# Kernel tuning notes

Measured on AMD Instinct MI355X. Metric: run time of the kernel, lower is better.

## Reference

```python
import jax, jax.numpy as jnp
import numpy as np

HEADS = 16
HEAD_DIM = 64
EMBED = HEADS * HEAD_DIM  # 1024
B, S = 2, 2048


def setup_inputs() -> dict:
    key = jax.random.key(0)
    ks = jax.random.split(key, 9)
    return {
        "value": jax.random.normal(ks[0], (B, S, EMBED), dtype=jnp.float32),
        "key": jax.random.normal(ks[1], (B, S, EMBED), dtype=jnp.float32),
        "query": jax.random.normal(ks[2], (B, S, EMBED), dtype=jnp.float32),
        "mask": jax.random.randint(ks[3], (B, 1, S, S), 0, 2, dtype=jnp.int32),
        "Wq": jax.random.normal(ks[4], (HEAD_DIM, HEAD_DIM), dtype=jnp.float32) * 0.02,
        "Wk": jax.random.normal(ks[5], (HEAD_DIM, HEAD_DIM), dtype=jnp.float32) * 0.02,
        "Wv": jax.random.normal(ks[6], (HEAD_DIM, HEAD_DIM), dtype=jnp.float32) * 0.02,
        "Wo": jax.random.normal(ks[7], (EMBED, EMBED), dtype=jnp.float32) * 0.02,
        "bo": jnp.zeros((EMBED,), dtype=jnp.float32),
    }


def reference(value, key, query, mask, Wq, Wk, Wv, Wo, bo):
    N, Lv = value.shape[0], value.shape[1]
    Lk, Lq = key.shape[1], query.shape[1]
    # Faithful to original: plain reshape (N, heads, len, head_dim), NOT transpose.
    v = value.reshape(N, HEADS, Lv, HEAD_DIM)
    k = key.reshape(N, HEADS, Lk, HEAD_DIM)
    q = query.reshape(N, HEADS, Lq, HEAD_DIM)
    # Per-head Linear (no bias): x @ W.T
    V = jnp.einsum('bhld,ed->bhle', v, Wv)
    K = jnp.einsum('bhld,ed->bhle', k, Wk)
    Q = jnp.einsum('bhld,ed->bhle', q, Wq)
    score = jnp.einsum('bhqd,bhkd->bhqk', Q, K)  # [B,H,Sq,Sk]
    score = jnp.where(mask == 0, jnp.float32(-1e20), score)
    # Faithful quirk: scale by sqrt(embed_size), not sqrt(head_dim)
    scale = jnp.float32(EMBED ** 0.5)
    attn = jax.nn.softmax(score / scale, axis=3)
    out = jnp.einsum('bhqk,bhkd->bhqd', attn, V).reshape(N, Lq, HEADS * HEAD_DIM)
    return out @ Wo.T + bo
```

## Files before the change

kernel.cpp:

```cpp
#include <hip/hip_runtime.h>
#include <hip/hip_bf16.h>
#include <cstdint>
#include <cstddef>

#define S_LEN 2048
#define N_HEADS 16
#define HD 64
#define EMB 1024
#define N_BATCH 2
#define N_BH (N_BATCH * N_HEADS)

typedef __attribute__((ext_vector_type(4))) float f32x4;
typedef __attribute__((ext_vector_type(8))) short short8;
typedef __attribute__((ext_vector_type(8))) _Float16 half8;
typedef __attribute__((ext_vector_type(2))) _Float16 half2v;

__device__ __forceinline__ f32x4 mfma16h(half8 a, half8 b, f32x4 c) {
    return __builtin_amdgcn_mfma_f32_16x16x32_f16(a, b, c, 0, 0, 0);
}

__device__ __forceinline__ unsigned pkh(float a, float b) {
    return __builtin_bit_cast(unsigned, __builtin_amdgcn_cvt_pkrtz(a, b));
}

#if __has_builtin(__builtin_amdgcn_exp2f)
__device__ __forceinline__ float fast_exp2(float x) { return __builtin_amdgcn_exp2f(x); }
#else
__device__ __forceinline__ float fast_exp2(float x) { return exp2f(x); }
#endif

__global__ __launch_bounds__(256) void prep_kernel(
    const float* __restrict__ q_in, const float* __restrict__ k_in,
    const float* __restrict__ v_in,
    const float* __restrict__ Wq, const float* __restrict__ Wk,
    const float* __restrict__ Wv, const float* __restrict__ Wo,
    const int* __restrict__ mask,
    short* __restrict__ Qb, short* __restrict__ Kb, short* __restrict__ Vt,
    short* __restrict__ Woh, unsigned long long* __restrict__ bits) {
    __shared__ short Al[64 * 72];
    __shared__ short Wl[64 * 72];
    __shared__ short Ol[64 * 72];
    int bx = blockIdx.x;
    int t = threadIdx.x;

    if (bx >= 3072) {
        if (bx < 11264) {
            int wid = ((bx - 3072) * 256 + t) >> 6;
            int lane = t & 63;
            const int* src = mask + (size_t)wid * 256 + lane;
            unsigned long long w0 = __ballot(src[0] != 0);
            unsigned long long w1 = __ballot(src[64] != 0);
            unsigned long long w2 = __ballot(src[128] != 0);
            unsigned long long w3 = __ballot(src[192] != 0);
            if (lane == 0) {
                unsigned long long* dst = bits + (size_t)wid * 4;
                dst[0] = w0; dst[1] = w1; dst[2] = w2; dst[3] = w3;
            }
        } else {
            int i = (bx - 11264) * 256 + t;
            f32x4 a = reinterpret_cast<const f32x4*>(Wo)[i * 2];
            f32x4 b = reinterpret_cast<const f32x4*>(Wo)[i * 2 + 1];
            uint4 u = { pkh(a.x, a.y), pkh(a.z, a.w), pkh(b.x, b.y), pkh(b.z, b.w) };
            reinterpret_cast<uint4*>(Woh)[i] = u;
        }
        return;
    }

    int rt = bx & 31;
    int bh = (bx >> 5) & 31;
    int tz = bx >> 10;
    const float* src = (tz == 0 ? q_in : tz == 1 ? k_in : v_in)
                       + (size_t)bh * S_LEN * HD + (size_t)rt * 64 * HD;
    const float* W = (tz == 0 ? Wq : tz == 1 ? Wk : Wv);

#pragma unroll
    for (int r = 0; r < 4; r++) {
        int f4 = t + 256 * r;
        int row = f4 >> 4;
        int c4 = (f4 & 15) * 4;
        f32x4 a = reinterpret_cast<const f32x4*>(src)[f4];
        uint2 ua = { pkh(a.x, a.y), pkh(a.z, a.w) };
        *reinterpret_cast<uint2*>(&Al[row * 72 + c4]) = ua;
        f32x4 w = reinterpret_cast<const f32x4*>(W)[f4];
        uint2 uw = { pkh(w.x, w.y), pkh(w.z, w.w) };
        *reinterpret_cast<uint2*>(&Wl[row * 72 + c4]) = uw;
    }
    __syncthreads();

    int wave = t >> 6, lane = t & 63, quad = lane >> 4, col = lane & 15;
    half8 a0 = *reinterpret_cast<const half8*>(&Al[(wave * 16 + col) * 72 + quad * 8]);
    half8 a1 = *reinterpret_cast<const half8*>(&Al[(wave * 16 + col) * 72 + 32 + quad * 8]);

    const float C1 = 0.04508422002777448f;
    float scl = (tz == 0) ? C1 : 1.0f;

    f32x4 acc[4];
#pragma unroll
    for (int jt = 0; jt < 4; jt++) {
        half8 b0 = *reinterpret_cast<const half8*>(&Wl[(jt * 16 + col) * 72 + quad * 8]);
        half8 b1 = *reinterpret_cast<const half8*>(&Wl[(jt * 16 + col) * 72 + 32 + quad * 8]);
        f32x4 c = {0.f, 0.f, 0.f, 0.f};
        c = mfma16h(a0, b0, c);
        c = mfma16h(a1, b1, c);
        acc[jt] = c;
    }
    __syncthreads();

    if (tz < 2) {
#pragma unroll
        for (int jt = 0; jt < 4; jt++)
#pragma unroll
            for (int i = 0; i < 4; i++)
                Ol[(wave * 16 + quad * 4 + i) * 72 + jt * 16 + col] =
                    __builtin_bit_cast(short, (_Float16)(acc[jt][i] * scl));
        __syncthreads();
        short* dst = (tz == 0 ? Qb : Kb) + (size_t)bh * S_LEN * HD + (size_t)rt * 64 * HD;
        int row = t >> 2, ck = (t & 3) * 16;
        short8 o0 = *reinterpret_cast<const short8*>(&Ol[row * 72 + ck]);
        short8 o1 = *reinterpret_cast<const short8*>(&Ol[row * 72 + ck + 8]);
        *reinterpret_cast<short8*>(&dst[row * 64 + ck]) = o0;
        *reinterpret_cast<short8*>(&dst[row * 64 + ck + 8]) = o1;
    } else {
#pragma unroll
        for (int jt = 0; jt < 4; jt++)
#pragma unroll
            for (int i = 0; i < 4; i++)
                Ol[(jt * 16 + col) * 72 + wave * 16 + quad * 4 + i] =
                    __builtin_bit_cast(short, (_Float16)acc[jt][i]);
        __syncthreads();
        short* dst = Vt + (size_t)bh * HD * S_LEN + rt * 64;
        int d = t >> 2, ck = (t & 3) * 16;
        short8 o0 = *reinterpret_cast<const short8*>(&Ol[d * 72 + ck]);
        short8 o1 = *reinterpret_cast<const short8*>(&Ol[d * 72 + ck + 8]);
        *reinterpret_cast<short8*>(&dst[(size_t)d * S_LEN + ck]) = o0;
        *reinterpret_cast<short8*>(&dst[(size_t)d * S_LEN + ck + 8]) = o1;
    }
}

__global__ __launch_bounds__(512, 4) void attn_kernel(
    const short* __restrict__ Qb, const short* __restrict__ Kb,
    const short* __restrict__ Vt, const unsigned long long* __restrict__ mbits,
    short* __restrict__ Xb) {
    int qt = blockIdx.x;
    int bh = blockIdx.y;
    int b = bh >> 4;
    int t = threadIdx.x, wave = t >> 6, lane = t & 63, quad = lane >> 4, col = lane & 15;

    __shared__ short Ks[64 * 64];
    __shared__ short Vs[64 * 64];
    __shared__ short Pl[8][16 * 72];
    short* Pw = &Pl[wave][0];

    const short* Qh = Qb + (size_t)bh * S_LEN * HD;
    const short* Kh = Kb + (size_t)bh * S_LEN * HD;
    const short* Vh = Vt + (size_t)bh * HD * S_LEN;
    int q0w = qt * 128 + wave * 16;
    int q = q0w + col;

    half8 qf0 = *reinterpret_cast<const half8*>(&Qh[(size_t)q * HD + quad * 8]);
    half8 qf1 = *reinterpret_cast<const half8*>(&Qh[(size_t)q * HD + 32 + quad * 8]);
    const unsigned long long* mrow = mbits + (size_t)(b * S_LEN + q) * 32;

    int r0 = t >> 3, cc = t & 7;
    int dst0 = r0 * 64 + ((cc ^ (r0 & 7)) * 8);
    const short* kg0 = Kh + r0 * HD + cc * 8;
    const short* vg0 = Vh + (size_t)r0 * S_LEN + cc * 8;

    short8 pk0 = *reinterpret_cast<const short8*>(kg0);
    short8 pv0 = *reinterpret_cast<const short8*>(vg0);
    *reinterpret_cast<short8*>(&Ks[dst0]) = pk0;
    *reinterpret_cast<short8*>(&Vs[dst0]) = pv0;
    __syncthreads();

    unsigned bs[4];
#pragma unroll
    for (int i = 0; i < 4; i++) bs[i] = 1u << (quad * 4 + i);
    half8 ones = { (_Float16)1.f, (_Float16)1.f, (_Float16)1.f, (_Float16)1.f,
                   (_Float16)1.f, (_Float16)1.f, (_Float16)1.f, (_Float16)1.f };

    int sw = quad ^ (col & 7);
    unsigned long long mw = mrow[0];

    f32x4 o[4];
    f32x4 l = {0.f, 0.f, 0.f, 0.f};
#pragma unroll
    for (int dt = 0; dt < 4; dt++) o[dt] = (f32x4){0.f, 0.f, 0.f, 0.f};

    for (int kt = 0; kt < 32; kt++) {
        unsigned long long mw_n;
        if (kt < 31) {
            pk0 = *reinterpret_cast<const short8*>(kg0 + (kt + 1) * 4096);
            pv0 = *reinterpret_cast<const short8*>(vg0 + (kt + 1) * 64);
            mw_n = mrow[kt + 1];
        }
        f32x4 s[4];
#pragma unroll
        for (int mt = 0; mt < 4; mt++) {
            const short* kbase = &Ks[(mt * 16 + col) * 64];
            half8 ka0 = *reinterpret_cast<const half8*>(&kbase[sw * 8]);
            half8 ka1 = *reinterpret_cast<const half8*>(&kbase[(sw ^ 4) * 8]);
            f32x4 c = {0.f, 0.f, 0.f, 0.f};
            c = mfma16h(ka0, qf0, c);
            c = mfma16h(ka1, qf1, c);
            s[mt] = c;
        }
#pragma unroll
        for (int mt = 0; mt < 4; mt++) {
            unsigned g = (unsigned)(mw >> (mt * 16));
            float p0 = fast_exp2((g & bs[0]) ? s[mt][0] : -200.0f);
            float p1 = fast_exp2((g & bs[1]) ? s[mt][1] : -200.0f);
            float p2 = fast_exp2((g & bs[2]) ? s[mt][2] : -200.0f);
            float p3 = fast_exp2((g & bs[3]) ? s[mt][3] : -200.0f);
            uint2 dw = { pkh(p0, p1), pkh(p2, p3) };
            *reinterpret_cast<uint2*>(&Pw[col * 72 + mt * 16 + quad * 4]) = dw;
        }
#pragma unroll
        for (int c = 0; c < 2; c++) {
            half8 pb = *reinterpret_cast<const half8*>(&Pw[col * 72 + c * 32 + quad * 8]);
            l = mfma16h(ones, pb, l);
#pragma unroll
            for (int dt = 0; dt < 4; dt++) {
                half8 va = *reinterpret_cast<const half8*>(
                    &Vs[(dt * 16 + col) * 64 + (((c * 4 + quad) ^ (col & 7)) * 8)]);
                o[dt] = mfma16h(va, pb, o[dt]);
            }
        }
        __syncthreads();
        if (kt < 31) {
            *reinterpret_cast<short8*>(&Ks[dst0]) = pk0;
            *reinterpret_cast<short8*>(&Vs[dst0]) = pv0;
            mw = mw_n;
            __syncthreads();
        }
    }

    float inv = 1.0f / l[0];
#pragma unroll
    for (int dt = 0; dt < 4; dt++) {
        uint2 dw = { pkh(o[dt][0] * inv, o[dt][1] * inv),
                     pkh(o[dt][2] * inv, o[dt][3] * inv) };
        *reinterpret_cast<uint2*>(&Pw[col * 72 + dt * 16 + quad * 4]) = dw;
    }
    int rr = lane >> 2, ck = (lane & 3) * 16;
    short8 x0 = *reinterpret_cast<const short8*>(&Pw[rr * 72 + ck]);
    short8 x1 = *reinterpret_cast<const short8*>(&Pw[rr * 72 + ck + 8]);
    short* Xrow = Xb + (size_t)bh * S_LEN * HD + (size_t)(q0w + rr) * HD;
    *reinterpret_cast<short8*>(&Xrow[ck]) = x0;
    *reinterpret_cast<short8*>(&Xrow[ck + 8]) = x1;
}

__global__ __launch_bounds__(256, 4) void final_kernel(
    const short* __restrict__ Xb, const short* __restrict__ Woh,
    const float* __restrict__ bo, float* __restrict__ out) {
    int nb = blockIdx.x;
    int mb = blockIdx.y;
    int t = threadIdx.x, wave = t >> 6, lane = t & 63, quad = lane >> 4, col = lane & 15;
    __shared__ short Xs[64 * 64];
    __shared__ short Ws[64 * 64];
    __shared__ float Olds[64 * 68];

    int m0 = mb * 64, n0 = nb * 64;
    int r0 = t >> 3, r1 = (t + 256) >> 3, cc = t & 7;
    int dst0 = r0 * 64 + ((cc ^ (r0 & 7)) * 8);
    int dst1 = r1 * 64 + ((cc ^ (r1 & 7)) * 8);
    const short* xg0 = Xb + (size_t)(m0 + r0) * EMB + cc * 8;
    const short* xg1 = Xb + (size_t)(m0 + r1) * EMB + cc * 8;
    const short* wg0 = Woh + (size_t)(n0 + r0) * EMB + cc * 8;
    const short* wg1 = Woh + (size_t)(n0 + r1) * EMB + cc * 8;

    short8 px0 = *reinterpret_cast<const short8*>(xg0);
    short8 px1 = *reinterpret_cast<const short8*>(xg1);
    short8 pw0 = *reinterpret_cast<const short8*>(wg0);
    short8 pw1 = *reinterpret_cast<const short8*>(wg1);
    *reinterpret_cast<short8*>(&Xs[dst0]) = px0;
    *reinterpret_cast<short8*>(&Xs[dst1]) = px1;
    *reinterpret_cast<short8*>(&Ws[dst0]) = pw0;
    *reinterpret_cast<short8*>(&Ws[dst1]) = pw1;
    __syncthreads();

    int sw = quad ^ (col & 7);
    f32x4 acc[4];
#pragma unroll
    for (int jt = 0; jt < 4; jt++) acc[jt] = (f32x4){0.f, 0.f, 0.f, 0.f};

    for (int s = 0; s < 16; s++) {
        if (s < 15) {
            px0 = *reinterpret_cast<const short8*>(xg0 + (s + 1) * 64);
            px1 = *reinterpret_cast<const short8*>(xg1 + (s + 1) * 64);
            pw0 = *reinterpret_cast<const short8*>(wg0 + (s + 1) * 64);
            pw1 = *reinterpret_cast<const short8*>(wg1 + (s + 1) * 64);
        }
        const short* arow = &Xs[(wave * 16 + col) * 64];
        half8 a0 = *reinterpret_cast<const half8*>(&arow[sw * 8]);
        half8 a1 = *reinterpret_cast<const half8*>(&arow[(sw ^ 4) * 8]);
#pragma unroll
        for (int jt = 0; jt < 4; jt++) {
            const short* brow = &Ws[(jt * 16 + col) * 64];
            half8 b0 = *reinterpret_cast<const half8*>(&brow[sw * 8]);
            half8 b1 = *reinterpret_cast<const half8*>(&brow[(sw ^ 4) * 8]);
            acc[jt] = mfma16h(a0, b0, acc[jt]);
            acc[jt] = mfma16h(a1, b1, acc[jt]);
        }
        __syncthreads();
        if (s < 15) {
            *reinterpret_cast<short8*>(&Xs[dst0]) = px0;
            *reinterpret_cast<short8*>(&Xs[dst1]) = px1;
            *reinterpret_cast<short8*>(&Ws[dst0]) = pw0;
            *reinterpret_cast<short8*>(&Ws[dst1]) = pw1;
            __syncthreads();
        }
    }

#pragma unroll
    for (int jt = 0; jt < 4; jt++)
#pragma unroll
        for (int i = 0; i < 4; i++)
            Olds[(wave * 16 + quad * 4 + i) * 68 + jt * 16 + col] = acc[jt][i];
    __syncthreads();
    int row = t >> 2, ck = (t & 3) * 16;
#pragma unroll
    for (int u = 0; u < 4; u++) {
        f32x4 v = *reinterpret_cast<const f32x4*>(&Olds[row * 68 + ck + u * 4]);
        f32x4 bb = *reinterpret_cast<const f32x4*>(&bo[n0 + ck + u * 4]);
        v.x += bb.x; v.y += bb.y; v.z += bb.z; v.w += bb.w;
        *reinterpret_cast<f32x4*>(&out[(size_t)(m0 + row) * EMB + n0 + ck + u * 4]) = v;
    }
}

extern "C" void kernel_launch(void* const* d_in, const int* in_sizes, int n_in,
                              void* d_out, int out_size, void* d_ws, size_t ws_size,
                              hipStream_t stream) {
    const float* value = (const float*)d_in[0];
    const float* key_  = (const float*)d_in[1];
    const float* query = (const float*)d_in[2];
    const int*   mask  = (const int*)d_in[3];
    const float* Wq = (const float*)d_in[4];
    const float* Wk = (const float*)d_in[5];
    const float* Wv = (const float*)d_in[6];
    const float* Wo = (const float*)d_in[7];
    const float* bo = (const float*)d_in[8];
    float* out = (float*)d_out;

    char* ws = (char*)d_ws;
    short* Qb  = (short*)(ws);
    short* Kb  = (short*)(ws + (size_t)8  * 1048576);
    short* Vt  = (short*)(ws + (size_t)16 * 1048576);
    short* Xb  = (short*)(ws + (size_t)24 * 1048576);
    short* Woh = (short*)(ws + (size_t)32 * 1048576);
    unsigned long long* mbits =
        (unsigned long long*)(ws + (size_t)34 * 1048576);

    prep_kernel<<<dim3(3072 + 8192 + 512), dim3(256), 0, stream>>>(
        query, key_, value, Wq, Wk, Wv, Wo, mask, Qb, Kb, Vt, Woh, mbits);
    attn_kernel<<<dim3(S_LEN / 128, N_BH), dim3(512), 0, stream>>>(Qb, Kb, Vt, mbits, Xb);
    final_kernel<<<dim3(EMB / 64, (N_BATCH * S_LEN) / 64), dim3(256), 0, stream>>>(
        Xb, Woh, bo, out);
}
```

Measured before the change: 205.8 us.

## Split KV tiles across wave halves with 32-row query tiles per wave

The attention kernel now gives each wave 32 query rows (two 16-row MFMA tiles) so every K and V fragment read from LDS feeds twice as many MFMAs. The 8 waves are split into two parity groups that process alternating 64-key tiles, with two K/V tiles staged per sync. The partial outputs and row sums are merged through shared memory at the end. This is meant to halve LDS traffic per FLOP and halve the number of barriers, at the cost of more registers, a larger shared-memory footprint, and a final cross-wave reduction.

```diff
diff --git a/kernel.cpp b/kernel.cpp
--- a/kernel.cpp
+++ b/kernel.cpp
@@ -145,31 +145,43 @@
     int bh = blockIdx.y;
     int b = bh >> 4;
     int t = threadIdx.x, wave = t >> 6, lane = t & 63, quad = lane >> 4, col = lane & 15;
-
-    __shared__ short Ks[64 * 64];
-    __shared__ short Vs[64 * 64];
-    __shared__ short Pl[8][16 * 72];
-    short* Pw = &Pl[wave][0];
+    int qg = wave & 3;
+    int par = wave >> 2;
+
+    __shared__ short smem[16384 + 8 * 32 * 72];
+    short* Pl = smem + 16384;
+    short* Pw = Pl + wave * (32 * 72);
+    const short* Kp = smem + par * 4096;
+    const short* Vp = smem + 8192 + par * 4096;
 
     const short* Qh = Qb + (size_t)bh * S_LEN * HD;
     const short* Kh = Kb + (size_t)bh * S_LEN * HD;
     const short* Vh = Vt + (size_t)bh * HD * S_LEN;
-    int q0w = qt * 128 + wave * 16;
-    int q = q0w + col;
-
-    half8 qf0 = *reinterpret_cast<const half8*>(&Qh[(size_t)q * HD + quad * 8]);
-    half8 qf1 = *reinterpret_cast<const half8*>(&Qh[(size_t)q * HD + 32 + quad * 8]);
-    const unsigned long long* mrow = mbits + (size_t)(b * S_LEN + q) * 32;
+    int q0 = qt * 128 + qg * 32;
+
+    half8 qf00 = *reinterpret_cast<const half8*>(&Qh[(size_t)(q0 + col) * HD + quad * 8]);
+    half8 qf01 = *reinterpret_cast<const half8*>(&Qh[(size_t)(q0 + col) * HD + 32 + quad * 8]);
+    half8 qf10 = *reinterpret_cast<const half8*>(&Qh[(size_t)(q0 + 16 + col) * HD + quad * 8]);
+    half8 qf11 = *reinterpret_cast<const half8*>(&Qh[(size_t)(q0 + 16 + col) * HD + 32 + quad * 8]);
+
+    const unsigned long long* mrow0 = mbits + (size_t)(b * S_LEN + q0 + col) * 32;
+    const unsigned long long* mrow1 = mbits + (size_t)(b * S_LEN + q0 + 16 + col) * 32;
 
     int r0 = t >> 3, cc = t & 7;
     int dst0 = r0 * 64 + ((cc ^ (r0 & 7)) * 8);
     const short* kg0 = Kh + r0 * HD + cc * 8;
     const short* vg0 = Vh + (size_t)r0 * S_LEN + cc * 8;
 
-    short8 pk0 = *reinterpret_cast<const short8*>(kg0);
-    short8 pv0 = *reinterpret_cast<const short8*>(vg0);
-    *reinterpret_cast<short8*>(&Ks[dst0]) = pk0;
-    *reinterpret_cast<short8*>(&Vs[dst0]) = pv0;
+    {
+        short8 a = *reinterpret_cast<const short8*>(kg0);
+        short8 b2 = *reinterpret_cast<const short8*>(kg0 + 4096);
+        short8 c = *reinterpret_cast<const short8*>(vg0);
+        short8 d = *reinterpret_cast<const short8*>(vg0 + 64);
+        *reinterpret_cast<short8*>(&smem[dst0]) = a;
+        *reinterpret_cast<short8*>(&smem[4096 + dst0]) = b2;
+        *reinterpret_cast<short8*>(&smem[8192 + dst0]) = c;
+        *reinterpret_cast<short8*>(&smem[12288 + dst0]) = d;
+    }
     __syncthreads();
 
     unsigned bs[4];
@@ -179,74 +191,124 @@
                    (_Float16)1.f, (_Float16)1.f, (_Float16)1.f, (_Float16)1.f };
 
     int sw = quad ^ (col & 7);
-    unsigned long long mw = mrow[0];
-
-    f32x4 o[4];
-    f32x4 l = {0.f, 0.f, 0.f, 0.f};
-#pragma unroll
-    for (int dt = 0; dt < 4; dt++) o[dt] = (f32x4){0.f, 0.f, 0.f, 0.f};
-
-    for (int kt = 0; kt < 32; kt++) {
-        unsigned long long mw_n;
-        if (kt < 31) {
-            pk0 = *reinterpret_cast<const short8*>(kg0 + (kt + 1) * 4096);
-            pv0 = *reinterpret_cast<const short8*>(vg0 + (kt + 1) * 64);
-            mw_n = mrow[kt + 1];
-        }
-        f32x4 s[4];
+    unsigned long long mw0 = mrow0[par];
+    unsigned long long mw1 = mrow1[par];
+
+    f32x4 o[4][2];
+    f32x4 l0 = {0.f, 0.f, 0.f, 0.f}, l1 = {0.f, 0.f, 0.f, 0.f};
+#pragma unroll
+    for (int dt = 0; dt < 4; dt++) {
+        o[dt][0] = (f32x4){0.f, 0.f, 0.f, 0.f};
+        o[dt][1] = (f32x4){0.f, 0.f, 0.f, 0.f};
+    }
+
+    for (int s = 0; s < 16; s++) {
+        short8 pk0, pk1, pv0, pv1;
+        unsigned long long mn0, mn1;
+        if (s < 15) {
+            pk0 = *reinterpret_cast<const short8*>(kg0 + (2 * s + 2) * 4096);
+            pk1 = *reinterpret_cast<const short8*>(kg0 + (2 * s + 3) * 4096);
+            pv0 = *reinterpret_cast<const short8*>(vg0 + (2 * s + 2) * 64);
+            pv1 = *reinterpret_cast<const short8*>(vg0 + (2 * s + 3) * 64);
+            mn0 = mrow0[2 * s + 2 + par];
+            mn1 = mrow1[2 * s + 2 + par];
+        }
 #pragma unroll
         for (int mt = 0; mt < 4; mt++) {
-            const short* kbase = &Ks[(mt * 16 + col) * 64];
+            const short* kbase = &Kp[(mt * 16 + col) * 64];
             half8 ka0 = *reinterpret_cast<const half8*>(&kbase[sw * 8]);
             half8 ka1 = *reinterpret_cast<const half8*>(&kbase[(sw ^ 4) * 8]);
-            f32x4 c = {0.f, 0.f, 0.f, 0.f};
-            c = mfma16h(ka0, qf0, c);
-            c = mfma16h(ka1, qf1, c);
-            s[mt] = c;
-        }
-#pragma unroll
-        for (int mt = 0; mt < 4; mt++) {
-            unsigned g = (unsigned)(mw >> (mt * 16));
-            float p0 = fast_exp2((g & bs[0]) ? s[mt][0] : -200.0f);
-            float p1 = fast_exp2((g & bs[1]) ? s[mt][1] : -200.0f);
-            float p2 = fast_exp2((g & bs[2]) ? s[mt][2] : -200.0f);
-            float p3 = fast_exp2((g & bs[3]) ? s[mt][3] : -200.0f);
-            uint2 dw = { pkh(p0, p1), pkh(p2, p3) };
-            *reinterpret_cast<uint2*>(&Pw[col * 72 + mt * 16 + quad * 4]) = dw;
+            f32x4 c0 = {0.f, 0.f, 0.f, 0.f};
+            f32x4 c1 = {0.f, 0.f, 0.f, 0.f};
+            c0 = mfma16h(ka0, qf00, c0);
+            c0 = mfma16h(ka1, qf01, c0);
+            c1 = mfma16h(ka0, qf10, c1);
+            c1 = mfma16h(ka1, qf11, c1);
+            unsigned g0 = (unsigned)(mw0 >> (mt * 16));
+            unsigned g1 = (unsigned)(mw1 >> (mt * 16));
+            float p00 = fast_exp2((g0 & bs[0]) ? c0[0] : -200.0f);
+            float p01 = fast_exp2((g0 & bs[1]) ? c0[1] : -200.0f);
+            float p02 = fast_exp2((g0 & bs[2]) ? c0[2] : -200.0f);
+            float p03 = fast_exp2((g0 & bs[3]) ? c0[3] : -200.0f);
+            uint2 dw0 = { pkh(p00, p01), pkh(p02, p03) };
+            *reinterpret_cast<uint2*>(&Pw[col * 72 + mt * 16 + quad * 4]) = dw0;
+            float p10 = fast_exp2((g1 & bs[0]) ? c1[0] : -200.0f);
+            float p11 = fast_exp2((g1 & bs[1]) ? c1[1] : -200.0f);
+            float p12 = fast_exp2((g1 & bs[2]) ? c1[2] : -200.0f);
+            float p13 = fast_exp2((g1 & bs[3]) ? c1[3] : -200.0f);
+            uint2 dw1 = { pkh(p10, p11), pkh(p12, p13) };
+            *reinterpret_cast<uint2*>(&Pw[(16 + col) * 72 + mt * 16 + quad * 4]) = dw1;
         }
 #pragma unroll
         for (int c = 0; c < 2; c++) {
-            half8 pb = *reinterpret_cast<const half8*>(&Pw[col * 72 + c * 32 + quad * 8]);
-            l = mfma16h(ones, pb, l);
+            half8 pb0 = *reinterpret_cast<const half8*>(&Pw[col * 72 + c * 32 + quad * 8]);
+            half8 pb1 = *reinterpret_cast<const half8*>(&Pw[(16 + col) * 72 + c * 32 + quad * 8]);
+            l0 = mfma16h(ones, pb0, l0);
+            l1 = mfma16h(ones, pb1, l1);
 #pragma unroll
             for (int dt = 0; dt < 4; dt++) {
                 half8 va = *reinterpret_cast<const half8*>(
-                    &Vs[(dt * 16 + col) * 64 + (((c * 4 + quad) ^ (col & 7)) * 8)]);
-                o[dt] = mfma16h(va, pb, o[dt]);
+                    &Vp[(dt * 16 + col) * 64 + (((c * 4 + quad) ^ (col & 7)) * 8)]);
+                o[dt][0] = mfma16h(va, pb0, o[dt][0]);
+                o[dt][1] = mfma16h(va, pb1, o[dt][1]);
             }
         }
         __syncthreads();
-        if (kt < 31) {
-            *reinterpret_cast<short8*>(&Ks[dst0]) = pk0;
-            *reinterpret_cast<short8*>(&Vs[dst0]) = pv0;
-            mw = mw_n;
+        if (s < 15) {
+            *reinterpret_cast<short8*>(&smem[dst0]) = pk0;
+            *reinterpret_cast<short8*>(&smem[4096 + dst0]) = pk1;
+            *reinterpret_cast<short8*>(&smem[8192 + dst0]) = pv0;
+            *reinterpret_cast<short8*>(&smem[12288 + dst0]) = pv1;
+            mw0 = mn0;
+            mw1 = mn1;
             __syncthreads();
         }
     }
 
-    float inv = 1.0f / l[0];
-#pragma unroll
-    for (int dt = 0; dt < 4; dt++) {
-        uint2 dw = { pkh(o[dt][0] * inv, o[dt][1] * inv),
-                     pkh(o[dt][2] * inv, o[dt][3] * inv) };
-        *reinterpret_cast<uint2*>(&Pw[col * 72 + dt * 16 + quad * 4]) = dw;
-    }
-    int rr = lane >> 2, ck = (lane & 3) * 16;
-    short8 x0 = *reinterpret_cast<const short8*>(&Pw[rr * 72 + ck]);
-    short8 x1 = *reinterpret_cast<const short8*>(&Pw[rr * 72 + ck + 8]);
-    short* Xrow = Xb + (size_t)bh * S_LEN * HD + (size_t)(q0w + rr) * HD;
-    *reinterpret_cast<short8*>(&Xrow[ck]) = x0;
-    *reinterpret_cast<short8*>(&Xrow[ck + 8]) = x1;
+    float* Obuf = (float*)smem;
+    float* Lbuf = (float*)(Pl + 4 * (32 * 72));
+    if (par == 1) {
+        float* ob = Obuf + qg * 2048 + lane * 32;
+#pragma unroll
+        for (int dt = 0; dt < 4; dt++) {
+            *reinterpret_cast<f32x4*>(&ob[((dt * 2 + 0) ^ (lane & 7)) * 4]) = o[dt][0];
+            *reinterpret_cast<f32x4*>(&ob[((dt * 2 + 1) ^ (lane & 7)) * 4]) = o[dt][1];
+        }
+        if (quad == 0) {
+            Lbuf[qg * 32 + col] = l0[0];
+            Lbuf[qg * 32 + 16 + col] = l1[0];
+        }
+    }
+    __syncthreads();
+    if (par == 0) {
+        float* ob = Obuf + qg * 2048 + lane * 32;
+        float inv0 = 1.0f / (l0[0] + Lbuf[qg * 32 + col]);
+        float inv1 = 1.0f / (l1[0] + Lbuf[qg * 32 + 16 + col]);
+#pragma unroll
+        for (int dt = 0; dt < 4; dt++) {
+            f32x4 a0 = *reinterpret_cast<const f32x4*>(&ob[((dt * 2 + 0) ^ (lane & 7)) * 4]);
+            f32x4 a1 = *reinterpret_cast<const f32x4*>(&ob[((dt * 2 + 1) ^ (lane & 7)) * 4]);
+            float v00 = (o[dt][0][0] + a0.x) * inv0, v01 = (o[dt][0][1] + a0.y) * inv0;
+            float v02 = (o[dt][0][2] + a0.z) * inv0, v03 = (o[dt][0][3] + a0.w) * inv0;
+            float v10 = (o[dt][1][0] + a1.x) * inv1, v11 = (o[dt][1][1] + a1.y) * inv1;
+            float v12 = (o[dt][1][2] + a1.z) * inv1, v13 = (o[dt][1][3] + a1.w) * inv1;
+            uint2 dw0 = { pkh(v00, v01), pkh(v02, v03) };
+            uint2 dw1 = { pkh(v10, v11), pkh(v12, v13) };
+            *reinterpret_cast<uint2*>(&Pw[col * 72 + dt * 16 + quad * 4]) = dw0;
+            *reinterpret_cast<uint2*>(&Pw[(16 + col) * 72 + dt * 16 + quad * 4]) = dw1;
+        }
+        int rr = lane >> 2, ckk = (lane & 3) * 16;
+        short* Xrow = Xb + (size_t)bh * S_LEN * HD + (size_t)(q0 + rr) * HD;
+        short8 x0 = *reinterpret_cast<const short8*>(&Pw[rr * 72 + ckk]);
+        short8 x1 = *reinterpret_cast<const short8*>(&Pw[rr * 72 + ckk + 8]);
+        *reinterpret_cast<short8*>(&Xrow[ckk]) = x0;
+        *reinterpret_cast<short8*>(&Xrow[ckk + 8]) = x1;
+        short* Xrow2 = Xrow + 16 * HD;
+        short8 y0 = *reinterpret_cast<const short8*>(&Pw[(16 + rr) * 72 + ckk]);
+        short8 y1 = *reinterpret_cast<const short8*>(&Pw[(16 + rr) * 72 + ckk + 8]);
+        *reinterpret_cast<short8*>(&Xrow2[ckk]) = y0;
+        *reinterpret_cast<short8*>(&Xrow2[ckk + 8]) = y1;
+    }
 }
 
 __global__ __launch_bounds__(256, 4) void final_kernel(
```

After: 202.3 us. About the same (-1.7%).
